# Performance work log

Hardware: AMD Instinct MI355X
Metric: run time of the kernel (lower is better)

Reference implementation:

```python
import jax, jax.numpy as jnp
import numpy as np

DIM = 768
HEADS = 12
HD = DIM // HEADS  # 64
BASE = 100.0


def rope_sincos(H, W):
    # DINOv3 RopePositionEmbedding: normalize_coords='separate', base=100.0
    dd = HD // 4
    periods = BASE ** (jnp.arange(dd, dtype=jnp.float32) / dd)          # [dd]
    ch = (jnp.arange(H, dtype=jnp.float32) + 0.5) / H                    # pixel centers
    cw = (jnp.arange(W, dtype=jnp.float32) + 0.5) / W
    cy, cx = jnp.meshgrid(ch, cw, indexing='ij')
    coords = 2.0 * jnp.stack([cy, cx], axis=-1).reshape(H * W, 2) - 1.0  # [N,2] in [-1,1]
    angles = 2.0 * jnp.pi * coords[:, :, None] / periods[None, None, :]  # [N,2,dd]
    angles = angles.reshape(H * W, 2 * dd)                               # [N, HD//2]
    angles = jnp.concatenate([angles, angles], axis=-1)                  # [N, HD]
    return jnp.sin(angles), jnp.cos(angles)


def rotate_half(t):
    t1, t2 = jnp.split(t, 2, axis=-1)
    return jnp.concatenate([-t2, t1], axis=-1)


def setup_inputs() -> dict:
    key = jax.random.key(0)
    k1, k2, k3 = jax.random.split(key, 3)
    B, H, W = 2, 48, 48
    x = jax.random.normal(k1, (B, H, W, DIM), dtype=jnp.float32)
    w_qkv = jax.random.normal(k2, (3 * DIM, DIM), dtype=jnp.float32) * 0.02
    b_qkv = jnp.zeros((3 * DIM,), dtype=jnp.float32)
    w_proj = jax.random.normal(k3, (DIM, DIM), dtype=jnp.float32) * 0.02
    b_proj = jnp.zeros((DIM,), dtype=jnp.float32)
    return {"x": x, "w_qkv": w_qkv, "b_qkv": b_qkv, "w_proj": w_proj, "b_proj": b_proj}


def reference(x, w_qkv, b_qkv, w_proj, b_proj):
    B, H, W, C = x.shape
    N = H * W
    xf = x.reshape(B, N, C)
    qkv = xf @ w_qkv.T + b_qkv                                   # [B,N,3C]
    qkv = qkv.reshape(B, N, 3, HEADS, HD).transpose(2, 0, 3, 1, 4)
    q, k, v = qkv[0], qkv[1], qkv[2]                              # [B,h,N,d]
    sin, cos = rope_sincos(H, W)                                  # [N,d]
    q = q * cos + rotate_half(q) * sin
    k = k * cos + rotate_half(k) * sin
    scale = HD ** -0.5
    attn = jax.nn.softmax(jnp.einsum('bhqd,bhkd->bhqk', q, k) * scale, axis=-1)
    o = jnp.einsum('bhqk,bhkd->bhqd', attn, v)                    # [B,h,N,d]
    o = o.transpose(0, 2, 1, 3).reshape(B, N, C)
    o = o @ w_proj.T + b_proj
    return o.reshape(B, H, W, C)
```

## Files before the change

### kernel.cpp

```cpp
#include <hip/hip_runtime.h>

#define BATCH 2
#define NSEQ 2304
#define DIM 768
#define HEADS 12
#define HD 64
#define M_TOK (BATCH * NSEQ)
#define LDSP 72
#define KP 72
#define BH (BATCH * HEADS)
#define KT_HALF (NSEQ / 64 / 2)

typedef __attribute__((ext_vector_type(8))) short bf16x8;
typedef __attribute__((ext_vector_type(8))) short short8v;
typedef __attribute__((ext_vector_type(4))) float f32x4;
typedef __fp16 fp16x2 __attribute__((ext_vector_type(2)));
typedef _Float16 half4 __attribute__((ext_vector_type(4)));
typedef _Float16 half8 __attribute__((ext_vector_type(8)));

#define QSCALE (0.125f * 1.44269504088896f)
#define LOG2_100_D16 0.41524101186092029f

__device__ __forceinline__ short f2bf(float f) {
    union { float f; unsigned u; } v; v.f = f;
    unsigned r = v.u + 0x7fffu + ((v.u >> 16) & 1u);
    return (short)(r >> 16);
}

__device__ __forceinline__ half8 cat4(half4 a, half4 b) {
    half8 r;
    r[0] = a.x; r[1] = a.y; r[2] = a.z; r[3] = a.w;
    r[4] = b.x; r[5] = b.y; r[6] = b.z; r[7] = b.w;
    return r;
}

#define CN1 (M_TOK * DIM / 4)
#define CN2 (3 * DIM * DIM / 4)
#define CN3 (DIM * DIM / 4)
__global__ void cvt_all_kernel(const float* __restrict__ x, const float* __restrict__ wq,
                               const float* __restrict__ wp,
                               short* __restrict__ xb, short* __restrict__ wqb,
                               short* __restrict__ wpb) {
    int i = blockIdx.x * 256 + threadIdx.x;
    const float* src; short* dst; int j;
    if (i < CN1)              { src = x;  dst = xb;  j = i; }
    else if (i < CN1 + CN2)   { src = wq; dst = wqb; j = i - CN1; }
    else                      { src = wp; dst = wpb; j = i - CN1 - CN2; }
    float4 v = reinterpret_cast<const float4*>(src)[j];
    short4 o;
    o.x = f2bf(v.x); o.y = f2bf(v.y); o.z = f2bf(v.z); o.w = f2bf(v.w);
    reinterpret_cast<short4*>(dst)[j] = o;
}

__global__ __launch_bounds__(256) void gemm_qkv_kernel(
    const short* __restrict__ A,
    const short* __restrict__ Bt,
    const float* __restrict__ bias,
    short* __restrict__ qb, short* __restrict__ kbuf, _Float16* __restrict__ vtb)
{
    __shared__ __align__(16) short At[2][128 * LDSP];
    __shared__ __align__(16) short Bl[2][128 * LDSP];
    const int m0 = blockIdx.x * 128, n0 = blockIdx.y * 128;
    const int tid = threadIdx.x, lane = tid & 63, wave = tid >> 6;
    const int quad = lane >> 4, l16 = lane & 15;
    const int wm = (wave >> 1) * 64, wn = (wave & 1) * 64;
    const int r = tid >> 1, c0 = (tid & 1) * 32;
    f32x4 acc[4][4] = {};

    {
        const uint4* ga = reinterpret_cast<const uint4*>(&A[(size_t)(m0 + r) * DIM + c0]);
        const uint4* gb = reinterpret_cast<const uint4*>(&Bt[(size_t)(n0 + r) * DIM + c0]);
        uint4 a0 = ga[0], a1 = ga[1], a2 = ga[2], a3 = ga[3];
        uint4 b0 = gb[0], b1 = gb[1], b2 = gb[2], b3 = gb[3];
        uint4* sa = reinterpret_cast<uint4*>(&At[0][r * LDSP + c0]);
        uint4* sb = reinterpret_cast<uint4*>(&Bl[0][r * LDSP + c0]);
        sa[0] = a0; sa[1] = a1; sa[2] = a2; sa[3] = a3;
        sb[0] = b0; sb[1] = b1; sb[2] = b2; sb[3] = b3;
    }

    int cur = 0;
    for (int k0 = 0; k0 < DIM; k0 += 64) {
        __syncthreads();
        uint4 a0, a1, a2, a3, b0, b1, b2, b3;
        const bool pre = (k0 + 64 < DIM);
        if (pre) {
            const uint4* ga = reinterpret_cast<const uint4*>(&A[(size_t)(m0 + r) * DIM + k0 + 64 + c0]);
            const uint4* gb = reinterpret_cast<const uint4*>(&Bt[(size_t)(n0 + r) * DIM + k0 + 64 + c0]);
            a0 = ga[0]; a1 = ga[1]; a2 = ga[2]; a3 = ga[3];
            b0 = gb[0]; b1 = gb[1]; b2 = gb[2]; b3 = gb[3];
        }
#pragma unroll
        for (int ks = 0; ks < 2; ++ks) {
            bf16x8 af[4], bf[4];
#pragma unroll
            for (int mt = 0; mt < 4; ++mt)
                af[mt] = *reinterpret_cast<const bf16x8*>(&At[cur][(wm + mt * 16 + l16) * LDSP + ks * 32 + quad * 8]);
#pragma unroll
            for (int nt = 0; nt < 4; ++nt)
                bf[nt] = *reinterpret_cast<const bf16x8*>(&Bl[cur][(wn + nt * 16 + l16) * LDSP + ks * 32 + quad * 8]);
#pragma unroll
            for (int mt = 0; mt < 4; ++mt)
#pragma unroll
                for (int nt = 0; nt < 4; ++nt)
                    acc[mt][nt] = __builtin_amdgcn_mfma_f32_16x16x32_bf16(af[mt], bf[nt], acc[mt][nt], 0, 0, 0);
        }
        if (pre) {
            uint4* sa = reinterpret_cast<uint4*>(&At[cur ^ 1][r * LDSP + c0]);
            uint4* sb = reinterpret_cast<uint4*>(&Bl[cur ^ 1][r * LDSP + c0]);
            sa[0] = a0; sa[1] = a1; sa[2] = a2; sa[3] = a3;
            sb[0] = b0; sb[1] = b1; sb[2] = b2; sb[3] = b3;
        }
        cur ^= 1;
    }

    const int which = (n0 + wn) / DIM;
    const int head = ((n0 + wn) % DIM) / HD;
    const int b = m0 / NSEQ;
    const int tokb = m0 % NSEQ + wm;
    if (which == 2) {
#pragma unroll
        for (int mt = 0; mt < 4; ++mt)
#pragma unroll
            for (int nt = 0; nt < 4; ++nt) {
                const int n = n0 + wn + nt * 16 + l16;
                const int d = nt * 16 + l16;
                const float bi = bias[n];
                const int tok0 = tokb + mt * 16 + quad * 4;
                half4 hv;
                hv.x = (_Float16)(acc[mt][nt][0] + bi);
                hv.y = (_Float16)(acc[mt][nt][1] + bi);
                hv.z = (_Float16)(acc[mt][nt][2] + bi);
                hv.w = (_Float16)(acc[mt][nt][3] + bi);
                *reinterpret_cast<half4*>(&vtb[((size_t)(b * HEADS + head) * HD + d) * NSEQ + tok0]) = hv;
            }
    } else {
        short* dst = (which == 0) ? qb : kbuf;
        const float qs = (which == 0) ? QSCALE : 1.0f;
        float bi[4];
#pragma unroll
        for (int nt = 0; nt < 4; ++nt) bi[nt] = bias[n0 + wn + nt * 16 + l16];
        const float invp = __builtin_amdgcn_exp2f(-(float)l16 * LOG2_100_D16);
#pragma unroll
        for (int mt = 0; mt < 4; ++mt) {
#pragma unroll
            for (int rg = 0; rg < 4; ++rg) {
                const int tok = tokb + mt * 16 + quad * 4 + rg;
                const int yy = tok / 48, xx = tok - yy * 48;
                const float ry = (2.0f * (yy + 0.5f) * (1.0f / 48.0f) - 1.0f) * invp;
                const float rx = (2.0f * (xx + 0.5f) * (1.0f / 48.0f) - 1.0f) * invp;
                const float sy = __builtin_amdgcn_sinf(ry), cy = __builtin_amdgcn_cosf(ry);
                const float sx = __builtin_amdgcn_sinf(rx), cx = __builtin_amdgcn_cosf(rx);
                const float a0 = acc[mt][0][rg] + bi[0];
                const float a1 = acc[mt][1][rg] + bi[1];
                const float a2 = acc[mt][2][rg] + bi[2];
                const float a3 = acc[mt][3][rg] + bi[3];
                short* rp = &dst[((size_t)(b * HEADS + head) * NSEQ + tok) * HD];
                rp[l16]      = f2bf((a0 * cy - a2 * sy) * qs);
                rp[32 + l16] = f2bf((a2 * cy + a0 * sy) * qs);
                rp[16 + l16] = f2bf((a1 * cx - a3 * sx) * qs);
                rp[48 + l16] = f2bf((a3 * cx + a1 * sx) * qs);
            }
        }
    }
}

__global__ __launch_bounds__(256, 2) void attn_kernel(
    const short* __restrict__ qb, const short* __restrict__ kb,
    const _Float16* __restrict__ vtb, _Float16* __restrict__ opart,
    float* __restrict__ lpart)
{
    __shared__ __align__(16) short    Kt[2][64 * KP];
    __shared__ __align__(16) _Float16 Vt[2][64 * KP];
    const int wg = blockIdx.x;
    const int xcd = wg & 7;
    const int slot = wg >> 3;
    const int slab = xcd * 6 + slot / 9;
    const int qt = slot % 9;
    const int kh = slab & 1;
    const int bh = slab >> 1;
    const int tid = threadIdx.x, lane = tid & 63, wave = tid >> 6;
    const int quad = lane >> 4, l16 = lane & 15;
    const int qrow0 = qt * 256 + wave * 64;
    const short* qbase = qb + (size_t)bh * NSEQ * HD;
    const short* kbase = kb + (size_t)bh * NSEQ * HD;
    const _Float16* vbase = vtb + (size_t)bh * HD * NSEQ;

    bf16x8 qf[4][2];
#pragma unroll
    for (int mt = 0; mt < 4; ++mt)
#pragma unroll
        for (int ks = 0; ks < 2; ++ks)
            qf[mt][ks] = *reinterpret_cast<const bf16x8*>(
                &qbase[(size_t)(qrow0 + mt * 16 + l16) * HD + ks * 32 + quad * 8]);

    half8 ones8;
#pragma unroll
    for (int j = 0; j < 8; ++j) ones8[j] = (_Float16)1.0f;

    f32x4 oacc[4][4] = {};
    f32x4 lacc[4] = {};

    const int r = tid >> 2, cq = (tid & 3) * 16;
    const int t0 = kh * KT_HALF;
    const short* kp = kbase + (size_t)(t0 * 64 + r) * HD + cq;
    const _Float16* vp = vbase + (size_t)r * NSEQ + t0 * 64 + cq;
    {
        const uint4* gk = reinterpret_cast<const uint4*>(kp);
        uint4 k0 = gk[0], k1 = gk[1];
        const uint4* gv = reinterpret_cast<const uint4*>(vp);
        uint4 v0 = gv[0], v1 = gv[1];
        uint4* sk = reinterpret_cast<uint4*>(&Kt[0][r * KP + cq]);
        sk[0] = k0; sk[1] = k1;
        uint4* sv = reinterpret_cast<uint4*>(&Vt[0][r * KP + cq]);
        sv[0] = v0; sv[1] = v1;
        kp += 64 * HD;
        vp += 64;
    }

    int cur = 0;
    for (int kt = 0; kt < KT_HALF; ++kt) {
        __syncthreads();
        uint4 k0, k1, v0, v1;
        const bool pre = (kt + 1 < KT_HALF);
        if (pre) {
            const uint4* gk = reinterpret_cast<const uint4*>(kp);
            k0 = gk[0]; k1 = gk[1];
            const uint4* gv = reinterpret_cast<const uint4*>(vp);
            v0 = gv[0]; v1 = gv[1];
            kp += 64 * HD;
            vp += 64;
        }

        bf16x8 kf[2][4];
#pragma unroll
        for (int ks = 0; ks < 2; ++ks)
#pragma unroll
            for (int nt = 0; nt < 4; ++nt)
                kf[ks][nt] = *reinterpret_cast<const bf16x8*>(
                    &Kt[cur][(nt * 16 + l16) * KP + ks * 32 + quad * 8]);
        half8 vf8[2][4];
#pragma unroll
        for (int n2 = 0; n2 < 2; ++n2)
#pragma unroll
            for (int dt = 0; dt < 4; ++dt) {
                half4 va = *reinterpret_cast<const half4*>(
                    &Vt[cur][(dt * 16 + l16) * KP + (2 * n2) * 16 + quad * 4]);
                half4 vb = *reinterpret_cast<const half4*>(
                    &Vt[cur][(dt * 16 + l16) * KP + (2 * n2 + 1) * 16 + quad * 4]);
                vf8[n2][dt] = cat4(va, vb);
            }

#pragma unroll
        for (int mt = 0; mt < 4; ++mt) {
            f32x4 sacc[4] = {};
#pragma unroll
            for (int ks = 0; ks < 2; ++ks)
#pragma unroll
                for (int nt = 0; nt < 4; ++nt)
                    sacc[nt] = __builtin_amdgcn_mfma_f32_16x16x32_bf16(
                        kf[ks][nt], qf[mt][ks], sacc[nt], 0, 0, 0);

            half8 pf8[2];
#pragma unroll
            for (int n2 = 0; n2 < 2; ++n2) {
                fp16x2 w0 = __builtin_amdgcn_cvt_pkrtz(
                    __builtin_amdgcn_exp2f(sacc[2 * n2][0]),
                    __builtin_amdgcn_exp2f(sacc[2 * n2][1]));
                fp16x2 w1 = __builtin_amdgcn_cvt_pkrtz(
                    __builtin_amdgcn_exp2f(sacc[2 * n2][2]),
                    __builtin_amdgcn_exp2f(sacc[2 * n2][3]));
                fp16x2 w2 = __builtin_amdgcn_cvt_pkrtz(
                    __builtin_amdgcn_exp2f(sacc[2 * n2 + 1][0]),
                    __builtin_amdgcn_exp2f(sacc[2 * n2 + 1][1]));
                fp16x2 w3 = __builtin_amdgcn_cvt_pkrtz(
                    __builtin_amdgcn_exp2f(sacc[2 * n2 + 1][2]),
                    __builtin_amdgcn_exp2f(sacc[2 * n2 + 1][3]));
                half8 p;
                p[0] = (_Float16)w0.x; p[1] = (_Float16)w0.y;
                p[2] = (_Float16)w1.x; p[3] = (_Float16)w1.y;
                p[4] = (_Float16)w2.x; p[5] = (_Float16)w2.y;
                p[6] = (_Float16)w3.x; p[7] = (_Float16)w3.y;
                pf8[n2] = p;
            }

#pragma unroll
            for (int n2 = 0; n2 < 2; ++n2)
                lacc[mt] = __builtin_amdgcn_mfma_f32_16x16x32_f16(
                    pf8[n2], ones8, lacc[mt], 0, 0, 0);
#pragma unroll
            for (int n2 = 0; n2 < 2; ++n2)
#pragma unroll
                for (int dt = 0; dt < 4; ++dt)
                    oacc[mt][dt] = __builtin_amdgcn_mfma_f32_16x16x32_f16(
                        pf8[n2], vf8[n2][dt], oacc[mt][dt], 0, 0, 0);
        }

        if (pre) {
            uint4* sk = reinterpret_cast<uint4*>(&Kt[cur ^ 1][r * KP + cq]);
            sk[0] = k0; sk[1] = k1;
            uint4* sv = reinterpret_cast<uint4*>(&Vt[cur ^ 1][r * KP + cq]);
            sv[0] = v0; sv[1] = v1;
        }
        cur ^= 1;
    }

    _Float16* ob2 = opart + (size_t)(kh * BH + bh) * NSEQ * HD;
    float* lp2 = lpart + (size_t)(kh * BH + bh) * NSEQ;
#pragma unroll
    for (int mt = 0; mt < 4; ++mt) {
#pragma unroll
        for (int dt = 0; dt < 4; ++dt)
#pragma unroll
            for (int rg = 0; rg < 4; ++rg) {
                int row = qrow0 + mt * 16 + quad * 4 + rg;
                ob2[(size_t)row * HD + dt * 16 + l16] = (_Float16)oacc[mt][dt][rg];
            }
        if (l16 == 0) {
#pragma unroll
            for (int rg = 0; rg < 4; ++rg)
                lp2[qrow0 + mt * 16 + quad * 4 + rg] = lacc[mt][rg];
        }
    }
}

__global__ __launch_bounds__(256) void gemm_proj_kernel(
    const _Float16* __restrict__ op,
    const float* __restrict__ lp,
    const short* __restrict__ Bt,
    const float* __restrict__ bias,
    float* __restrict__ out)
{
    __shared__ __align__(16) short At[64 * LDSP];
    __shared__ __align__(16) short Bl[64 * LDSP];
    const int m0 = blockIdx.x * 64, n0 = blockIdx.y * 64;
    const int tid = threadIdx.x, lane = tid & 63, wave = tid >> 6;
    const int quad = lane >> 4, l16 = lane & 15;
    const int wm = (wave >> 1) * 32, wn = (wave & 1) * 32;
    const int r = tid >> 2, cs = (tid & 3) * 16;
    const int b = m0 / NSEQ;
    const int tok = m0 % NSEQ + r;
    f32x4 acc[2][2] = {};

    for (int k0 = 0; k0 < DIM; k0 += 64) {
        const int h = k0 >> 6;
        const size_t pb = (size_t)(b * HEADS + h) * NSEQ + tok;
        const float l0 = lp[pb], l1 = lp[(size_t)BH * NSEQ + pb];
        const float inv = __builtin_amdgcn_rcpf(l0 + l1);
        const half8* o0 = reinterpret_cast<const half8*>(&op[pb * HD + cs]);
        const half8* o1 = reinterpret_cast<const half8*>(&op[(size_t)BH * NSEQ * HD + pb * HD + cs]);
        half8 p0 = o0[0], p1 = o0[1], q0 = o1[0], q1 = o1[1];
        const uint4* gb = reinterpret_cast<const uint4*>(&Bt[(size_t)(n0 + r) * DIM + k0 + cs]);
        uint4 bw0 = gb[0], bw1 = gb[1];
        short8v s0, s1;
#pragma unroll
        for (int j = 0; j < 8; ++j) {
            s0[j] = f2bf(((float)p0[j] + (float)q0[j]) * inv);
            s1[j] = f2bf(((float)p1[j] + (float)q1[j]) * inv);
        }
        *reinterpret_cast<short8v*>(&At[r * LDSP + cs]) = s0;
        *reinterpret_cast<short8v*>(&At[r * LDSP + cs + 8]) = s1;
        uint4* sb = reinterpret_cast<uint4*>(&Bl[r * LDSP + cs]);
        sb[0] = bw0; sb[1] = bw1;
        __syncthreads();
#pragma unroll
        for (int ks = 0; ks < 2; ++ks) {
            bf16x8 af[2], bf[2];
#pragma unroll
            for (int mt = 0; mt < 2; ++mt)
                af[mt] = *reinterpret_cast<const bf16x8*>(&At[(wm + mt * 16 + l16) * LDSP + ks * 32 + quad * 8]);
#pragma unroll
            for (int nt = 0; nt < 2; ++nt)
                bf[nt] = *reinterpret_cast<const bf16x8*>(&Bl[(wn + nt * 16 + l16) * LDSP + ks * 32 + quad * 8]);
#pragma unroll
            for (int mt = 0; mt < 2; ++mt)
#pragma unroll
                for (int nt = 0; nt < 2; ++nt)
                    acc[mt][nt] = __builtin_amdgcn_mfma_f32_16x16x32_bf16(af[mt], bf[nt], acc[mt][nt], 0, 0, 0);
        }
        __syncthreads();
    }

#pragma unroll
    for (int mt = 0; mt < 2; ++mt)
#pragma unroll
        for (int nt = 0; nt < 2; ++nt) {
            const int n = n0 + wn + nt * 16 + l16;
            const float bi = bias[n];
#pragma unroll
            for (int rg = 0; rg < 4; ++rg) {
                const int m = m0 + wm + mt * 16 + quad * 4 + rg;
                out[(size_t)m * DIM + n] = acc[mt][nt][rg] + bi;
            }
        }
}

extern "C" void kernel_launch(void* const* d_in, const int* in_sizes, int n_in,
                              void* d_out, int out_size, void* d_ws, size_t ws_size,
                              hipStream_t stream) {
    const float* x      = (const float*)d_in[0];
    const float* w_qkv  = (const float*)d_in[1];
    const float* b_qkv  = (const float*)d_in[2];
    const float* w_proj = (const float*)d_in[3];
    const float* b_proj = (const float*)d_in[4];
    float* out = (float*)d_out;

    short* xb     = (short*)d_ws;
    short* wqkvb  = xb + (size_t)M_TOK * DIM;
    short* wprojb = wqkvb + (size_t)3 * DIM * DIM;
    short* qb     = wprojb + (size_t)DIM * DIM;
    short* kb     = qb + (size_t)BH * NSEQ * HD;
    short* vtb    = kb + (size_t)BH * NSEQ * HD;
    short* opart  = vtb + (size_t)BH * NSEQ * HD;
    float* lpart  = (float*)(opart + (size_t)2 * BH * NSEQ * HD);

    cvt_all_kernel<<<(CN1 + CN2 + CN3) / 256, 256, 0, stream>>>(
        x, w_qkv, w_proj, xb, wqkvb, wprojb);

    dim3 g1(M_TOK / 128, 3 * DIM / 128);
    gemm_qkv_kernel<<<g1, 256, 0, stream>>>(xb, wqkvb, b_qkv, qb, kb, (_Float16*)vtb);

    attn_kernel<<<dim3(9 * 2 * BH), 256, 0, stream>>>(qb, kb, (const _Float16*)vtb,
                                                      (_Float16*)opart, lpart);

    gemm_proj_kernel<<<dim3(M_TOK / 64, DIM / 64), 256, 0, stream>>>(
        (const _Float16*)opart, lpart, wprojb, b_proj, out);
}
```

Before: 170.6 us.

## Load K/V fragments directly from global into registers, single-wave attention blocks

Result: slower. 222.2 us (+30.2%).

```diff
diff --git a/kernel.cpp b/kernel.cpp
--- a/kernel.cpp
+++ b/kernel.cpp
@@ -7,7 +7,6 @@
 #define HD 64
 #define M_TOK (BATCH * NSEQ)
 #define LDSP 72
-#define KP 72
 #define BH (BATCH * HEADS)
 #define KT_HALF (NSEQ / 64 / 2)
 
@@ -164,23 +163,95 @@
     }
 }
 
-__global__ __launch_bounds__(256, 2) void attn_kernel(
+__device__ __forceinline__ void load_k(bf16x8 (&kf)[2][4], const short* kl) {
+#pragma unroll
+    for (int ks = 0; ks < 2; ++ks)
+#pragma unroll
+        for (int nt = 0; nt < 4; ++nt)
+            kf[ks][nt] = *reinterpret_cast<const bf16x8*>(kl + nt * 16 * HD + ks * 32);
+}
+
+__device__ __forceinline__ void load_v(half8 (&vf)[2][4], const _Float16* vl) {
+#pragma unroll
+    for (int n2 = 0; n2 < 2; ++n2)
+#pragma unroll
+        for (int dt = 0; dt < 4; ++dt) {
+            half4 a = *reinterpret_cast<const half4*>(vl + (size_t)dt * 16 * NSEQ + (2 * n2) * 16);
+            half4 b = *reinterpret_cast<const half4*>(vl + (size_t)dt * 16 * NSEQ + (2 * n2 + 1) * 16);
+            vf[n2][dt] = cat4(a, b);
+        }
+}
+
+__device__ __forceinline__ void compute_tile(
+    const bf16x8 (&kf)[2][4], const half8 (&vf)[2][4],
+    const bf16x8 (&qf)[4][2], half8 ones8,
+    f32x4 (&oacc)[4][4], f32x4 (&lacc)[4])
+{
+#pragma unroll
+    for (int mt = 0; mt < 4; ++mt) {
+        f32x4 sacc[4] = {};
+        __builtin_amdgcn_s_setprio(1);
+#pragma unroll
+        for (int ks = 0; ks < 2; ++ks)
+#pragma unroll
+            for (int nt = 0; nt < 4; ++nt)
+                sacc[nt] = __builtin_amdgcn_mfma_f32_16x16x32_bf16(
+                    kf[ks][nt], qf[mt][ks], sacc[nt], 0, 0, 0);
+        __builtin_amdgcn_s_setprio(0);
+
+        half8 pf8[2];
+#pragma unroll
+        for (int n2 = 0; n2 < 2; ++n2) {
+            fp16x2 w0 = __builtin_amdgcn_cvt_pkrtz(
+                __builtin_amdgcn_exp2f(sacc[2 * n2][0]),
+                __builtin_amdgcn_exp2f(sacc[2 * n2][1]));
+            fp16x2 w1 = __builtin_amdgcn_cvt_pkrtz(
+                __builtin_amdgcn_exp2f(sacc[2 * n2][2]),
+                __builtin_amdgcn_exp2f(sacc[2 * n2][3]));
+            fp16x2 w2 = __builtin_amdgcn_cvt_pkrtz(
+                __builtin_amdgcn_exp2f(sacc[2 * n2 + 1][0]),
+                __builtin_amdgcn_exp2f(sacc[2 * n2 + 1][1]));
+            fp16x2 w3 = __builtin_amdgcn_cvt_pkrtz(
+                __builtin_amdgcn_exp2f(sacc[2 * n2 + 1][2]),
+                __builtin_amdgcn_exp2f(sacc[2 * n2 + 1][3]));
+            half8 p;
+            p[0] = (_Float16)w0.x; p[1] = (_Float16)w0.y;
+            p[2] = (_Float16)w1.x; p[3] = (_Float16)w1.y;
+            p[4] = (_Float16)w2.x; p[5] = (_Float16)w2.y;
+            p[6] = (_Float16)w3.x; p[7] = (_Float16)w3.y;
+            pf8[n2] = p;
+        }
+
+        __builtin_amdgcn_s_setprio(1);
+#pragma unroll
+        for (int n2 = 0; n2 < 2; ++n2)
+            lacc[mt] = __builtin_amdgcn_mfma_f32_16x16x32_f16(
+                pf8[n2], ones8, lacc[mt], 0, 0, 0);
+#pragma unroll
+        for (int n2 = 0; n2 < 2; ++n2)
+#pragma unroll
+            for (int dt = 0; dt < 4; ++dt)
+                oacc[mt][dt] = __builtin_amdgcn_mfma_f32_16x16x32_f16(
+                    pf8[n2], vf[n2][dt], oacc[mt][dt], 0, 0, 0);
+        __builtin_amdgcn_s_setprio(0);
+    }
+}
+
+__global__ __launch_bounds__(64, 2) void attn_kernel(
     const short* __restrict__ qb, const short* __restrict__ kb,
     const _Float16* __restrict__ vtb, _Float16* __restrict__ opart,
     float* __restrict__ lpart)
 {
-    __shared__ __align__(16) short    Kt[2][64 * KP];
-    __shared__ __align__(16) _Float16 Vt[2][64 * KP];
     const int wg = blockIdx.x;
     const int xcd = wg & 7;
     const int slot = wg >> 3;
-    const int slab = xcd * 6 + slot / 9;
-    const int qt = slot % 9;
+    const int slab = xcd * 6 + slot / 36;
+    const int inner = slot % 36;
     const int kh = slab & 1;
     const int bh = slab >> 1;
-    const int tid = threadIdx.x, lane = tid & 63, wave = tid >> 6;
+    const int lane = threadIdx.x & 63;
     const int quad = lane >> 4, l16 = lane & 15;
-    const int qrow0 = qt * 256 + wave * 64;
+    const int qrow0 = inner * 64;
     const short* qbase = qb + (size_t)bh * NSEQ * HD;
     const short* kbase = kb + (size_t)bh * NSEQ * HD;
     const _Float16* vbase = vtb + (size_t)bh * HD * NSEQ;
@@ -200,108 +271,26 @@
     f32x4 oacc[4][4] = {};
     f32x4 lacc[4] = {};
 
-    const int r = tid >> 2, cq = (tid & 3) * 16;
     const int t0 = kh * KT_HALF;
-    const short* kp = kbase + (size_t)(t0 * 64 + r) * HD + cq;
-    const _Float16* vp = vbase + (size_t)r * NSEQ + t0 * 64 + cq;
-    {
-        const uint4* gk = reinterpret_cast<const uint4*>(kp);
-        uint4 k0 = gk[0], k1 = gk[1];
-        const uint4* gv = reinterpret_cast<const uint4*>(vp);
-        uint4 v0 = gv[0], v1 = gv[1];
-        uint4* sk = reinterpret_cast<uint4*>(&Kt[0][r * KP + cq]);
-        sk[0] = k0; sk[1] = k1;
-        uint4* sv = reinterpret_cast<uint4*>(&Vt[0][r * KP + cq]);
-        sv[0] = v0; sv[1] = v1;
-        kp += 64 * HD;
-        vp += 64;
-    }
-
-    int cur = 0;
-    for (int kt = 0; kt < KT_HALF; ++kt) {
-        __syncthreads();
-        uint4 k0, k1, v0, v1;
-        const bool pre = (kt + 1 < KT_HALF);
-        if (pre) {
-            const uint4* gk = reinterpret_cast<const uint4*>(kp);
-            k0 = gk[0]; k1 = gk[1];
-            const uint4* gv = reinterpret_cast<const uint4*>(vp);
-            v0 = gv[0]; v1 = gv[1];
-            kp += 64 * HD;
-            vp += 64;
-        }
-
-        bf16x8 kf[2][4];
-#pragma unroll
-        for (int ks = 0; ks < 2; ++ks)
-#pragma unroll
-            for (int nt = 0; nt < 4; ++nt)
-                kf[ks][nt] = *reinterpret_cast<const bf16x8*>(
-                    &Kt[cur][(nt * 16 + l16) * KP + ks * 32 + quad * 8]);
-        half8 vf8[2][4];
-#pragma unroll
-        for (int n2 = 0; n2 < 2; ++n2)
-#pragma unroll
-            for (int dt = 0; dt < 4; ++dt) {
-                half4 va = *reinterpret_cast<const half4*>(
-                    &Vt[cur][(dt * 16 + l16) * KP + (2 * n2) * 16 + quad * 4]);
-                half4 vb = *reinterpret_cast<const half4*>(
-                    &Vt[cur][(dt * 16 + l16) * KP + (2 * n2 + 1) * 16 + quad * 4]);
-                vf8[n2][dt] = cat4(va, vb);
-            }
-
-#pragma unroll
-        for (int mt = 0; mt < 4; ++mt) {
-            f32x4 sacc[4] = {};
-#pragma unroll
-            for (int ks = 0; ks < 2; ++ks)
-#pragma unroll
-                for (int nt = 0; nt < 4; ++nt)
-                    sacc[nt] = __builtin_amdgcn_mfma_f32_16x16x32_bf16(
-                        kf[ks][nt], qf[mt][ks], sacc[nt], 0, 0, 0);
-
-            half8 pf8[2];
-#pragma unroll
-            for (int n2 = 0; n2 < 2; ++n2) {
-                fp16x2 w0 = __builtin_amdgcn_cvt_pkrtz(
-                    __builtin_amdgcn_exp2f(sacc[2 * n2][0]),
-                    __builtin_amdgcn_exp2f(sacc[2 * n2][1]));
-                fp16x2 w1 = __builtin_amdgcn_cvt_pkrtz(
-                    __builtin_amdgcn_exp2f(sacc[2 * n2][2]),
-                    __builtin_amdgcn_exp2f(sacc[2 * n2][3]));
-                fp16x2 w2 = __builtin_amdgcn_cvt_pkrtz(
-                    __builtin_amdgcn_exp2f(sacc[2 * n2 + 1][0]),
-                    __builtin_amdgcn_exp2f(sacc[2 * n2 + 1][1]));
-                fp16x2 w3 = __builtin_amdgcn_cvt_pkrtz(
-                    __builtin_amdgcn_exp2f(sacc[2 * n2 + 1][2]),
-                    __builtin_amdgcn_exp2f(sacc[2 * n2 + 1][3]));
-                half8 p;
-                p[0] = (_Float16)w0.x; p[1] = (_Float16)w0.y;
-                p[2] = (_Float16)w1.x; p[3] = (_Float16)w1.y;
-                p[4] = (_Float16)w2.x; p[5] = (_Float16)w2.y;
-                p[6] = (_Float16)w3.x; p[7] = (_Float16)w3.y;
-                pf8[n2] = p;
-            }
-
-#pragma unroll
-            for (int n2 = 0; n2 < 2; ++n2)
-                lacc[mt] = __builtin_amdgcn_mfma_f32_16x16x32_f16(
-                    pf8[n2], ones8, lacc[mt], 0, 0, 0);
-#pragma unroll
-            for (int n2 = 0; n2 < 2; ++n2)
-#pragma unroll
-                for (int dt = 0; dt < 4; ++dt)
-                    oacc[mt][dt] = __builtin_amdgcn_mfma_f32_16x16x32_f16(
-                        pf8[n2], vf8[n2][dt], oacc[mt][dt], 0, 0, 0);
-        }
-
-        if (pre) {
-            uint4* sk = reinterpret_cast<uint4*>(&Kt[cur ^ 1][r * KP + cq]);
-            sk[0] = k0; sk[1] = k1;
-            uint4* sv = reinterpret_cast<uint4*>(&Vt[cur ^ 1][r * KP + cq]);
-            sv[0] = v0; sv[1] = v1;
-        }
-        cur ^= 1;
+    const short* kl = kbase + (size_t)(t0 * 64 + l16) * HD + quad * 8;
+    const _Float16* vl = vbase + (size_t)l16 * NSEQ + t0 * 64 + quad * 4;
+
+    bf16x8 kfA[2][4], kfB[2][4];
+    half8 vf[2][4];
+
+    load_k(kfA, kl);
+
+    for (int kt = 0; kt < KT_HALF; kt += 2) {
+        load_v(vf, vl);  vl += 64;
+        load_k(kfB, kl + 64 * HD);
+        compute_tile(kfA, vf, qf, ones8, oacc, lacc);
+
+        load_v(vf, vl);  vl += 64;
+        if (kt + 2 < KT_HALF)
+            load_k(kfA, kl + 2 * 64 * HD);
+        compute_tile(kfB, vf, qf, ones8, oacc, lacc);
+
+        kl += 2 * 64 * HD;
     }
 
     _Float16* ob2 = opart + (size_t)(kh * BH + bh) * NSEQ * HD;
@@ -419,7 +408,7 @@
     dim3 g1(M_TOK / 128, 3 * DIM / 128);
     gemm_qkv_kernel<<<g1, 256, 0, stream>>>(xb, wqkvb, b_qkv, qb, kb, (_Float16*)vtb);
 
-    attn_kernel<<<dim3(9 * 2 * BH), 256, 0, stream>>>(qb, kb, (const _Float16*)vtb,
+    attn_kernel<<<dim3(36 * 2 * BH), 64, 0, stream>>>(qb, kb, (const _Float16*)vtb,
                                                       (_Float16*)opart, lpart);
 
     gemm_proj_kernel<<<dim3(M_TOK / 64, DIM / 64), 256, 0, stream>>>(
```

## Permute V tile in LDS for 128-bit reads and software-pipeline QK with exp/PV

Applied to the files above, without the earlier changes.

Measured after the change: 167.4 us. About the same (-1.9%).

```diff
diff --git a/kernel.cpp b/kernel.cpp
--- a/kernel.cpp
+++ b/kernel.cpp
@@ -25,13 +25,6 @@
     union { float f; unsigned u; } v; v.f = f;
     unsigned r = v.u + 0x7fffu + ((v.u >> 16) & 1u);
     return (short)(r >> 16);
-}
-
-__device__ __forceinline__ half8 cat4(half4 a, half4 b) {
-    half8 r;
-    r[0] = a.x; r[1] = a.y; r[2] = a.z; r[3] = a.w;
-    r[4] = b.x; r[5] = b.y; r[6] = b.z; r[7] = b.w;
-    return r;
 }
 
 #define CN1 (M_TOK * DIM / 4)
@@ -162,6 +155,47 @@
             }
         }
     }
+}
+
+__device__ __forceinline__ void qk16(f32x4 (&s)[4], const bf16x8 (&kf)[2][4],
+                                     const bf16x8 (&q2)[2]) {
+#pragma unroll
+    for (int nt = 0; nt < 4; ++nt) s[nt] = f32x4{0.f, 0.f, 0.f, 0.f};
+#pragma unroll
+    for (int ks = 0; ks < 2; ++ks)
+#pragma unroll
+        for (int nt = 0; nt < 4; ++nt)
+            s[nt] = __builtin_amdgcn_mfma_f32_16x16x32_bf16(kf[ks][nt], q2[ks], s[nt], 0, 0, 0);
+}
+
+__device__ __forceinline__ void exp_pv(const f32x4 (&s)[4], const half8 (&vf8)[2][4],
+                                       half8 ones8, f32x4 (&omt)[4], f32x4& lmt) {
+    half8 pf8[2];
+#pragma unroll
+    for (int n2 = 0; n2 < 2; ++n2) {
+        fp16x2 w0 = __builtin_amdgcn_cvt_pkrtz(
+            __builtin_amdgcn_exp2f(s[2 * n2][0]), __builtin_amdgcn_exp2f(s[2 * n2][1]));
+        fp16x2 w1 = __builtin_amdgcn_cvt_pkrtz(
+            __builtin_amdgcn_exp2f(s[2 * n2][2]), __builtin_amdgcn_exp2f(s[2 * n2][3]));
+        fp16x2 w2 = __builtin_amdgcn_cvt_pkrtz(
+            __builtin_amdgcn_exp2f(s[2 * n2 + 1][0]), __builtin_amdgcn_exp2f(s[2 * n2 + 1][1]));
+        fp16x2 w3 = __builtin_amdgcn_cvt_pkrtz(
+            __builtin_amdgcn_exp2f(s[2 * n2 + 1][2]), __builtin_amdgcn_exp2f(s[2 * n2 + 1][3]));
+        half8 p;
+        p[0] = (_Float16)w0.x; p[1] = (_Float16)w0.y;
+        p[2] = (_Float16)w1.x; p[3] = (_Float16)w1.y;
+        p[4] = (_Float16)w2.x; p[5] = (_Float16)w2.y;
+        p[6] = (_Float16)w3.x; p[7] = (_Float16)w3.y;
+        pf8[n2] = p;
+    }
+#pragma unroll
+    for (int n2 = 0; n2 < 2; ++n2)
+        lmt = __builtin_amdgcn_mfma_f32_16x16x32_f16(pf8[n2], ones8, lmt, 0, 0, 0);
+#pragma unroll
+    for (int n2 = 0; n2 < 2; ++n2)
+#pragma unroll
+        for (int dt = 0; dt < 4; ++dt)
+            omt[dt] = __builtin_amdgcn_mfma_f32_16x16x32_f16(pf8[n2], vf8[n2][dt], omt[dt], 0, 0, 0);
 }
 
 __global__ __launch_bounds__(256, 2) void attn_kernel(
@@ -200,7 +234,8 @@
     f32x4 oacc[4][4] = {};
     f32x4 lacc[4] = {};
 
-    const int r = tid >> 2, cq = (tid & 3) * 16;
+    const int r = tid >> 2, tq = tid & 3, cq = tq * 16;
+    const int vdst = r * KP + 32 * (tq >> 1) + 4 * (tq & 1);
     const int t0 = kh * KT_HALF;
     const short* kp = kbase + (size_t)(t0 * 64 + r) * HD + cq;
     const _Float16* vp = vbase + (size_t)r * NSEQ + t0 * 64 + cq;
@@ -211,8 +246,11 @@
         uint4 v0 = gv[0], v1 = gv[1];
         uint4* sk = reinterpret_cast<uint4*>(&Kt[0][r * KP + cq]);
         sk[0] = k0; sk[1] = k1;
-        uint4* sv = reinterpret_cast<uint4*>(&Vt[0][r * KP + cq]);
-        sv[0] = v0; sv[1] = v1;
+        _Float16* vb = &Vt[0][vdst];
+        *reinterpret_cast<uint2*>(vb +  0) = make_uint2(v0.x, v0.y);
+        *reinterpret_cast<uint2*>(vb +  8) = make_uint2(v0.z, v0.w);
+        *reinterpret_cast<uint2*>(vb + 16) = make_uint2(v1.x, v1.y);
+        *reinterpret_cast<uint2*>(vb + 24) = make_uint2(v1.z, v1.w);
         kp += 64 * HD;
         vp += 64;
     }
@@ -242,64 +280,30 @@
 #pragma unroll
         for (int n2 = 0; n2 < 2; ++n2)
 #pragma unroll
-            for (int dt = 0; dt < 4; ++dt) {
-                half4 va = *reinterpret_cast<const half4*>(
-                    &Vt[cur][(dt * 16 + l16) * KP + (2 * n2) * 16 + quad * 4]);
-                half4 vb = *reinterpret_cast<const half4*>(
-                    &Vt[cur][(dt * 16 + l16) * KP + (2 * n2 + 1) * 16 + quad * 4]);
-                vf8[n2][dt] = cat4(va, vb);
-            }
-
-#pragma unroll
-        for (int mt = 0; mt < 4; ++mt) {
-            f32x4 sacc[4] = {};
-#pragma unroll
-            for (int ks = 0; ks < 2; ++ks)
-#pragma unroll
-                for (int nt = 0; nt < 4; ++nt)
-                    sacc[nt] = __builtin_amdgcn_mfma_f32_16x16x32_bf16(
-                        kf[ks][nt], qf[mt][ks], sacc[nt], 0, 0, 0);
-
-            half8 pf8[2];
-#pragma unroll
-            for (int n2 = 0; n2 < 2; ++n2) {
-                fp16x2 w0 = __builtin_amdgcn_cvt_pkrtz(
-                    __builtin_amdgcn_exp2f(sacc[2 * n2][0]),
-                    __builtin_amdgcn_exp2f(sacc[2 * n2][1]));
-                fp16x2 w1 = __builtin_amdgcn_cvt_pkrtz(
-                    __builtin_amdgcn_exp2f(sacc[2 * n2][2]),
-                    __builtin_amdgcn_exp2f(sacc[2 * n2][3]));
-                fp16x2 w2 = __builtin_amdgcn_cvt_pkrtz(
-                    __builtin_amdgcn_exp2f(sacc[2 * n2 + 1][0]),
-                    __builtin_amdgcn_exp2f(sacc[2 * n2 + 1][1]));
-                fp16x2 w3 = __builtin_amdgcn_cvt_pkrtz(
-                    __builtin_amdgcn_exp2f(sacc[2 * n2 + 1][2]),
-                    __builtin_amdgcn_exp2f(sacc[2 * n2 + 1][3]));
-                half8 p;
-                p[0] = (_Float16)w0.x; p[1] = (_Float16)w0.y;
-                p[2] = (_Float16)w1.x; p[3] = (_Float16)w1.y;
-                p[4] = (_Float16)w2.x; p[5] = (_Float16)w2.y;
-                p[6] = (_Float16)w3.x; p[7] = (_Float16)w3.y;
-                pf8[n2] = p;
-            }
-
-#pragma unroll
-            for (int n2 = 0; n2 < 2; ++n2)
-                lacc[mt] = __builtin_amdgcn_mfma_f32_16x16x32_f16(
-                    pf8[n2], ones8, lacc[mt], 0, 0, 0);
-#pragma unroll
-            for (int n2 = 0; n2 < 2; ++n2)
-#pragma unroll
-                for (int dt = 0; dt < 4; ++dt)
-                    oacc[mt][dt] = __builtin_amdgcn_mfma_f32_16x16x32_f16(
-                        pf8[n2], vf8[n2][dt], oacc[mt][dt], 0, 0, 0);
+            for (int dt = 0; dt < 4; ++dt)
+                vf8[n2][dt] = *reinterpret_cast<const half8*>(
+                    &Vt[cur][(dt * 16 + l16) * KP + 32 * n2 + 8 * quad]);
+
+        {
+            f32x4 sa[4], sb[4];
+            qk16(sa, kf, qf[0]);
+            qk16(sb, kf, qf[1]);
+            exp_pv(sa, vf8, ones8, oacc[0], lacc[0]);
+            qk16(sa, kf, qf[2]);
+            exp_pv(sb, vf8, ones8, oacc[1], lacc[1]);
+            qk16(sb, kf, qf[3]);
+            exp_pv(sa, vf8, ones8, oacc[2], lacc[2]);
+            exp_pv(sb, vf8, ones8, oacc[3], lacc[3]);
         }
 
         if (pre) {
             uint4* sk = reinterpret_cast<uint4*>(&Kt[cur ^ 1][r * KP + cq]);
             sk[0] = k0; sk[1] = k1;
-            uint4* sv = reinterpret_cast<uint4*>(&Vt[cur ^ 1][r * KP + cq]);
-            sv[0] = v0; sv[1] = v1;
+            _Float16* vb = &Vt[cur ^ 1][vdst];
+            *reinterpret_cast<uint2*>(vb +  0) = make_uint2(v0.x, v0.y);
+            *reinterpret_cast<uint2*>(vb +  8) = make_uint2(v0.z, v0.w);
+            *reinterpret_cast<uint2*>(vb + 16) = make_uint2(v1.x, v1.y);
+            *reinterpret_cast<uint2*>(vb + 24) = make_uint2(v1.z, v1.w);
         }
         cur ^= 1;
     }
```

## Split attention query tiles across eight waves and permute V in LDS

Applied to the files above, without the earlier changes.

After: 165.4 us. 3.0% less time.

```diff
diff --git a/kernel.cpp b/kernel.cpp
--- a/kernel.cpp
+++ b/kernel.cpp
@@ -25,13 +25,6 @@
     union { float f; unsigned u; } v; v.f = f;
     unsigned r = v.u + 0x7fffu + ((v.u >> 16) & 1u);
     return (short)(r >> 16);
-}
-
-__device__ __forceinline__ half8 cat4(half4 a, half4 b) {
-    half8 r;
-    r[0] = a.x; r[1] = a.y; r[2] = a.z; r[3] = a.w;
-    r[4] = b.x; r[5] = b.y; r[6] = b.z; r[7] = b.w;
-    return r;
 }
 
 #define CN1 (M_TOK * DIM / 4)
@@ -164,7 +157,7 @@
     }
 }
 
-__global__ __launch_bounds__(256, 2) void attn_kernel(
+__global__ __launch_bounds__(512, 4) void attn_kernel(
     const short* __restrict__ qb, const short* __restrict__ kb,
     const _Float16* __restrict__ vtb, _Float16* __restrict__ opart,
     float* __restrict__ lpart)
@@ -180,14 +173,14 @@
     const int bh = slab >> 1;
     const int tid = threadIdx.x, lane = tid & 63, wave = tid >> 6;
     const int quad = lane >> 4, l16 = lane & 15;
-    const int qrow0 = qt * 256 + wave * 64;
+    const int qrow0 = qt * 256 + wave * 32;
     const short* qbase = qb + (size_t)bh * NSEQ * HD;
     const short* kbase = kb + (size_t)bh * NSEQ * HD;
     const _Float16* vbase = vtb + (size_t)bh * HD * NSEQ;
 
-    bf16x8 qf[4][2];
-#pragma unroll
-    for (int mt = 0; mt < 4; ++mt)
+    bf16x8 qf[2][2];
+#pragma unroll
+    for (int mt = 0; mt < 2; ++mt)
 #pragma unroll
         for (int ks = 0; ks < 2; ++ks)
             qf[mt][ks] = *reinterpret_cast<const bf16x8*>(
@@ -197,22 +190,23 @@
 #pragma unroll
     for (int j = 0; j < 8; ++j) ones8[j] = (_Float16)1.0f;
 
-    f32x4 oacc[4][4] = {};
-    f32x4 lacc[4] = {};
-
-    const int r = tid >> 2, cq = (tid & 3) * 16;
-    const int t0 = kh * KT_HALF;
-    const short* kp = kbase + (size_t)(t0 * 64 + r) * HD + cq;
-    const _Float16* vp = vbase + (size_t)r * NSEQ + t0 * 64 + cq;
+    f32x4 oacc[2][4] = {};
+    f32x4 lacc[2] = {};
+
+    const int rk = tid >> 3, ck = (tid & 7) * 8;
+    const int wv = tid & 7;
+    const int vdst = rk * KP + 32 * (wv >> 2) + 16 * (wv & 1) + 4 * ((wv >> 1) & 1);
+    const int t0 = kh * (NSEQ / 2);
+    const short* kp = kbase + (size_t)(t0 + rk) * HD + ck;
+    const _Float16* vp = vbase + (size_t)rk * NSEQ + t0 + wv * 8;
+
     {
-        const uint4* gk = reinterpret_cast<const uint4*>(kp);
-        uint4 k0 = gk[0], k1 = gk[1];
-        const uint4* gv = reinterpret_cast<const uint4*>(vp);
-        uint4 v0 = gv[0], v1 = gv[1];
-        uint4* sk = reinterpret_cast<uint4*>(&Kt[0][r * KP + cq]);
-        sk[0] = k0; sk[1] = k1;
-        uint4* sv = reinterpret_cast<uint4*>(&Vt[0][r * KP + cq]);
-        sv[0] = v0; sv[1] = v1;
+        uint4 k0 = *reinterpret_cast<const uint4*>(kp);
+        uint4 v0 = *reinterpret_cast<const uint4*>(vp);
+        *reinterpret_cast<uint4*>(&Kt[0][rk * KP + ck]) = k0;
+        _Float16* vb = &Vt[0][vdst];
+        *reinterpret_cast<uint2*>(vb + 0) = make_uint2(v0.x, v0.y);
+        *reinterpret_cast<uint2*>(vb + 8) = make_uint2(v0.z, v0.w);
         kp += 64 * HD;
         vp += 64;
     }
@@ -220,13 +214,11 @@
     int cur = 0;
     for (int kt = 0; kt < KT_HALF; ++kt) {
         __syncthreads();
-        uint4 k0, k1, v0, v1;
+        uint4 k0, v0;
         const bool pre = (kt + 1 < KT_HALF);
         if (pre) {
-            const uint4* gk = reinterpret_cast<const uint4*>(kp);
-            k0 = gk[0]; k1 = gk[1];
-            const uint4* gv = reinterpret_cast<const uint4*>(vp);
-            v0 = gv[0]; v1 = gv[1];
+            k0 = *reinterpret_cast<const uint4*>(kp);
+            v0 = *reinterpret_cast<const uint4*>(vp);
             kp += 64 * HD;
             vp += 64;
         }
@@ -242,16 +234,12 @@
 #pragma unroll
         for (int n2 = 0; n2 < 2; ++n2)
 #pragma unroll
-            for (int dt = 0; dt < 4; ++dt) {
-                half4 va = *reinterpret_cast<const half4*>(
-                    &Vt[cur][(dt * 16 + l16) * KP + (2 * n2) * 16 + quad * 4]);
-                half4 vb = *reinterpret_cast<const half4*>(
-                    &Vt[cur][(dt * 16 + l16) * KP + (2 * n2 + 1) * 16 + quad * 4]);
-                vf8[n2][dt] = cat4(va, vb);
-            }
-
-#pragma unroll
-        for (int mt = 0; mt < 4; ++mt) {
+            for (int dt = 0; dt < 4; ++dt)
+                vf8[n2][dt] = *reinterpret_cast<const half8*>(
+                    &Vt[cur][(dt * 16 + l16) * KP + 32 * n2 + 8 * quad]);
+
+#pragma unroll
+        for (int mt = 0; mt < 2; ++mt) {
             f32x4 sacc[4] = {};
 #pragma unroll
             for (int ks = 0; ks < 2; ++ks)
@@ -296,10 +284,10 @@
         }
 
         if (pre) {
-            uint4* sk = reinterpret_cast<uint4*>(&Kt[cur ^ 1][r * KP + cq]);
-            sk[0] = k0; sk[1] = k1;
-            uint4* sv = reinterpret_cast<uint4*>(&Vt[cur ^ 1][r * KP + cq]);
-            sv[0] = v0; sv[1] = v1;
+            *reinterpret_cast<uint4*>(&Kt[cur ^ 1][rk * KP + ck]) = k0;
+            _Float16* vb = &Vt[cur ^ 1][vdst];
+            *reinterpret_cast<uint2*>(vb + 0) = make_uint2(v0.x, v0.y);
+            *reinterpret_cast<uint2*>(vb + 8) = make_uint2(v0.z, v0.w);
         }
         cur ^= 1;
     }
@@ -307,7 +295,7 @@
     _Float16* ob2 = opart + (size_t)(kh * BH + bh) * NSEQ * HD;
     float* lp2 = lpart + (size_t)(kh * BH + bh) * NSEQ;
 #pragma unroll
-    for (int mt = 0; mt < 4; ++mt) {
+    for (int mt = 0; mt < 2; ++mt) {
 #pragma unroll
         for (int dt = 0; dt < 4; ++dt)
 #pragma unroll
@@ -419,7 +407,7 @@
     dim3 g1(M_TOK / 128, 3 * DIM / 128);
     gemm_qkv_kernel<<<g1, 256, 0, stream>>>(xb, wqkvb, b_qkv, qb, kb, (_Float16*)vtb);
 
-    attn_kernel<<<dim3(9 * 2 * BH), 256, 0, stream>>>(qb, kb, (const _Float16*)vtb,
+    attn_kernel<<<dim3(9 * 2 * BH), 512, 0, stream>>>(qb, kb, (const _Float16*)vtb,
                                                       (_Float16*)opart, lpart);
 
     gemm_proj_kernel<<<dim3(M_TOK / 64, DIM / 64), 256, 0, stream>>>(
```
